# Kernel tuning notes

Hardware: AMD Instinct MI355X
Metric: run time of the kernel (lower is better)

Reference implementation:

```python
import jax, jax.numpy as jnp
import numpy as np

N = 100_000      # nodes
E = 1_600_000    # edges (before self loops)
IN, HID, OUT, H = 128, 32, 40, 4
NEG_SLOPE = 0.2  # PyG GATConv default


def setup_inputs() -> dict:
    key = jax.random.key(0)
    ks = jax.random.split(key, 10)
    s = 0.1  # small init scale (glorot-like)
    return {
        "x": jax.random.normal(ks[0], (N, IN), jnp.float32),
        "edge_index": jax.random.randint(ks[1], (2, E), 0, N, dtype=jnp.int32),
        "W1": jax.random.normal(ks[2], (IN, H * HID), jnp.float32) * s,
        "att_src1": jax.random.normal(ks[3], (H, HID), jnp.float32) * s,
        "att_dst1": jax.random.normal(ks[4], (H, HID), jnp.float32) * s,
        "b1": jnp.zeros((H * HID,), jnp.float32),
        "W2": jax.random.normal(ks[5], (H * HID, H * OUT), jnp.float32) * s,
        "att_src2": jax.random.normal(ks[6], (H, OUT), jnp.float32) * s,
        "att_dst2": jax.random.normal(ks[7], (H, OUT), jnp.float32) * s,
        "b2": jnp.zeros((OUT,), jnp.float32),
    }


def gat_layer(x, src, dst, W, a_src, a_dst, b, concat):
    """PyG-style GATConv: edge (src -> dst), softmax over incoming edges per dst."""
    Hh, C = a_src.shape
    h = (x @ W).reshape(-1, Hh, C)                      # [N, H, C]
    s_src = jnp.einsum('nhc,hc->nh', h, a_src)           # [N, H]
    s_dst = jnp.einsum('nhc,hc->nh', h, a_dst)           # [N, H]
    e = jax.nn.leaky_relu(s_src[src] + s_dst[dst], NEG_SLOPE)  # [E', H]
    m = jax.ops.segment_max(e, dst, num_segments=N)      # per-dst max for stability
    p = jnp.exp(e - m[dst])
    z = jax.ops.segment_sum(p, dst, num_segments=N)
    alpha = p / z[dst]                                    # segment softmax [E', H]
    out = jax.ops.segment_sum(alpha[:, :, None] * h[src], dst, num_segments=N)  # [N,H,C]
    out = out.reshape(-1, Hh * C) if concat else out.mean(axis=1)
    return out + b


def reference(x, edge_index, W1, att_src1, att_dst1, b1, W2, att_src2, att_dst2, b2):
    loops = jnp.arange(N, dtype=edge_index.dtype)        # PyG add_self_loops=True
    src = jnp.concatenate([edge_index[0], loops])
    dst = jnp.concatenate([edge_index[1], loops])
    h = jax.nn.elu(gat_layer(x, src, dst, W1, att_src1, att_dst1, b1, concat=True))
    h = gat_layer(h, src, dst, W2, att_src2, att_dst2, b2, concat=False)
    return jax.nn.log_softmax(h, axis=1)
```

## Files before the change

kernel.cpp:

```cpp
#include <hip/hip_runtime.h>
#include <hip/hip_bf16.h>

#define N_NODES 100000
#define M_PAD   100096
#define N_EDGES 1600000
#define E_TOT   (N_EDGES + N_NODES)
#define NEG_SLOPE 0.2f

#define G_NODES 128
#define BUCKETS ((N_NODES + G_NODES - 1) / G_NODES)
#define REP 512
#define SLICE ((E_TOT + REP - 1) / REP)
#define GB1 (M_PAD / 128)
#define CVTW_ELEMS (128 * 128 + 128 * 160)
#define CVTW_BLOCKS ((CVTW_ELEMS + 255) / 256)

typedef __attribute__((ext_vector_type(8))) short s16x8;
typedef __attribute__((ext_vector_type(4))) float f32x4;
typedef __attribute__((ext_vector_type(2))) float f32x2;

__device__ __forceinline__ float lo16(unsigned u) { return __uint_as_float(u << 16); }
__device__ __forceinline__ float hi16(unsigned u) { return __uint_as_float(u & 0xffff0000u); }

__device__ __forceinline__ short f2bf(float f) {
    __hip_bfloat16 b = __float2bfloat16(f);
    return *(short*)&b;
}


__device__ void slice_count_body(const int* __restrict__ ei, int* __restrict__ cnt, int r) {
    __shared__ int h[BUCKETS];
    for (int i = threadIdx.x; i < BUCKETS; i += 256) h[i] = 0;
    __syncthreads();
    int lo = r * SLICE, hi = min(lo + SLICE, E_TOT);
    for (int e = lo + threadIdx.x; e < hi; e += 256) {
        int d = (e < N_EDGES) ? ei[N_EDGES + e] : e - N_EDGES;
        atomicAdd(&h[d >> 7], 1);
    }
    __syncthreads();
    for (int i = threadIdx.x; i < BUCKETS; i += 256)
        cnt[(size_t)r * BUCKETS + i] = h[i];
}

__device__ void col_scan256_body(int* __restrict__ cnt, int* __restrict__ bsum, int b) {
    __shared__ int lds[256];
    int tid = threadIdx.x;
    int v0 = cnt[(size_t)(2 * tid) * BUCKETS + b];
    int v1 = cnt[(size_t)(2 * tid + 1) * BUCKETS + b];
    int s = v0 + v1;
    lds[tid] = s;
    __syncthreads();
    for (int off = 1; off < 256; off <<= 1) {
        int t = (tid >= off) ? lds[tid - off] : 0;
        __syncthreads();
        lds[tid] += t;
        __syncthreads();
    }
    int excl = lds[tid] - s;
    cnt[(size_t)(2 * tid) * BUCKETS + b]     = excl;
    cnt[(size_t)(2 * tid + 1) * BUCKETS + b] = excl + v0;
    if (tid == 255) bsum[b] = lds[255];
}

__device__ void bucket_scan_body(const int* __restrict__ bsum, int* __restrict__ boff) {
    __shared__ int lds[1024];
    int tid = threadIdx.x;
    int v = (tid < BUCKETS) ? bsum[tid] : 0;
    lds[tid] = v;
    __syncthreads();
    for (int off = 1; off < 1024; off <<= 1) {
        int t = (tid >= off) ? lds[tid - off] : 0;
        __syncthreads();
        lds[tid] += t;
        __syncthreads();
    }
    if (tid < BUCKETS) boff[tid] = lds[tid] - v;
    if (tid == 0) boff[BUCKETS] = E_TOT;
}

__global__ __launch_bounds__(256) void bucket_scatter_kernel(const int* __restrict__ ei,
                                                             const int* __restrict__ colx,
                                                             const int* __restrict__ boff,
                                                             int* __restrict__ tmp) {
    __shared__ int lcur[BUCKETS];
    int r = blockIdx.x;
    for (int i = threadIdx.x; i < BUCKETS; i += 256)
        lcur[i] = boff[i] + colx[(size_t)r * BUCKETS + i];
    __syncthreads();
    int lo = r * SLICE, hi = min(lo + SLICE, E_TOT);
    for (int e = lo + threadIdx.x; e < hi; e += 256) {
        int s, d;
        if (e < N_EDGES) { s = ei[e]; d = ei[N_EDGES + e]; }
        else             { s = d = e - N_EDGES; }
        int pos = atomicAdd(&lcur[d >> 7], 1);
        tmp[pos] = (s << 7) | (d & (G_NODES - 1));
    }
}

__global__ __launch_bounds__(256) void bucket_build_kernel(const int* __restrict__ tmp,
                                                           const int* __restrict__ boff,
                                                           int* __restrict__ rowptr,
                                                           int* __restrict__ csr) {
    __shared__ int hcnt[G_NODES];
    __shared__ int hoff[G_NODES];
    int b = blockIdx.x;
    int base = boff[b], cnt = boff[b + 1] - base;
    int tid = threadIdx.x;
    if (tid < G_NODES) hcnt[tid] = 0;
    __syncthreads();
    for (int i = tid; i < cnt; i += 256)
        atomicAdd(&hcnt[tmp[base + i] & (G_NODES - 1)], 1);
    __syncthreads();
    if (tid < G_NODES) hoff[tid] = hcnt[tid];
    __syncthreads();
    for (int off = 1; off < G_NODES; off <<= 1) {
        int t = (tid < G_NODES && tid >= off) ? hoff[tid - off] : 0;
        __syncthreads();
        if (tid < G_NODES) hoff[tid] += t;
        __syncthreads();
    }
    if (tid < G_NODES) {
        int excl = hoff[tid] - hcnt[tid];
        int node = b * G_NODES + tid;
        if (node < N_NODES) rowptr[node] = base + excl;
        hcnt[tid] = excl;
    }
    __syncthreads();
    for (int i = tid; i < cnt; i += 256) {
        int v = tmp[base + i];
        int pos = base + atomicAdd(&hcnt[v & (G_NODES - 1)], 1);
        csr[pos] = v >> 7;
    }
    if (b == 0 && tid < 8) csr[E_TOT + tid] = 0;
    if (b == 0 && tid == 0) rowptr[N_NODES] = E_TOT;
}


__device__ void cvt_w_body(const float* __restrict__ W1, __hip_bfloat16* __restrict__ W1t,
                           const float* __restrict__ W2, __hip_bfloat16* __restrict__ W2t,
                           int idx) {
    if (idx < 128 * 128) {
        int k = idx >> 7, n = idx & 127;
        W1t[n * 128 + k] = __float2bfloat16(W1[idx]);
    } else if (idx < CVTW_ELEMS) {
        int i = idx - 128 * 128;
        int k = i / 160, n = i - k * 160;
        W2t[n * 128 + k] = __float2bfloat16(W2[i]);
    }
}

__device__ void gemm1_body(const float* __restrict__ A, const __hip_bfloat16* __restrict__ Bt,
                           unsigned char* __restrict__ Cq, int bid) {
    constexpr int NCOLS = 128;
    constexpr int CG = NCOLS / 32;
    int wid = threadIdx.x >> 6;
    int lane = threadIdx.x & 63;
    int wr = wid >> 1, wc = wid & 1;
    int l15 = lane & 15, lk = lane >> 4;

    s16x8 bfrag[CG][4];
    #pragma unroll
    for (int cg = 0; cg < CG; ++cg) {
        int col = wc * (NCOLS / 2) + cg * 16 + l15;
        #pragma unroll
        for (int ks = 0; ks < 4; ++ks)
            bfrag[cg][ks] = *(const s16x8*)&Bt[col * 128 + ks * 32 + lk * 8];
    }
    int rowblk = bid * 128;
    #pragma unroll
    for (int st = 0; st < 4; ++st) {
        int rbase = rowblk + st * 32 + wr * 16;
        int row = rbase + l15;
        bool ok = row < N_NODES;
        s16x8 afrag[4];
        #pragma unroll
        for (int ks = 0; ks < 4; ++ks) {
            if (ok) {
                float4 a0 = *(const float4*)&A[(size_t)row * 128 + ks * 32 + lk * 8];
                float4 a1 = *(const float4*)&A[(size_t)row * 128 + ks * 32 + lk * 8 + 4];
                s16x8 af;
                af[0] = f2bf(a0.x); af[1] = f2bf(a0.y); af[2] = f2bf(a0.z); af[3] = f2bf(a0.w);
                af[4] = f2bf(a1.x); af[5] = f2bf(a1.y); af[6] = f2bf(a1.z); af[7] = f2bf(a1.w);
                afrag[ks] = af;
            } else {
                afrag[ks] = (s16x8){0,0,0,0,0,0,0,0};
            }
        }
        f32x4 acc[CG];
        #pragma unroll
        for (int cg = 0; cg < CG; ++cg) acc[cg] = (f32x4){0.f, 0.f, 0.f, 0.f};
        #pragma unroll
        for (int ks = 0; ks < 4; ++ks) {
            #pragma unroll
            for (int cg = 0; cg < CG; ++cg)
                acc[cg] = __builtin_amdgcn_mfma_f32_16x16x32_bf16(afrag[ks], bfrag[cg][ks], acc[cg], 0, 0, 0);
        }
        #pragma unroll
        for (int cg = 0; cg < CG; ++cg) {
            int c = wc * (NCOLS / 2) + cg * 16 + l15;
            unsigned w01 = __builtin_amdgcn_cvt_pk_fp8_f32(acc[cg][0], acc[cg][1], 0, false);
            unsigned w23 = __builtin_amdgcn_cvt_pk_fp8_f32(acc[cg][2], acc[cg][3], 0, false);
            size_t base = (size_t)(rbase + lk * 4) * NCOLS + c;
            Cq[base]             = (unsigned char)(w01 & 0xff);
            Cq[base + NCOLS]     = (unsigned char)((w01 >> 8) & 0xff);
            Cq[base + 2 * NCOLS] = (unsigned char)(w23 & 0xff);
            Cq[base + 3 * NCOLS] = (unsigned char)((w23 >> 8) & 0xff);
        }
    }
}

template<int NCOLS>
__global__ __launch_bounds__(256) void mfma_gemm_kernel(const __hip_bfloat16* __restrict__ A,
                                                        const __hip_bfloat16* __restrict__ Bt,
                                                        unsigned char* __restrict__ Cq) {
    constexpr int CG = NCOLS / 32;
    int wid = threadIdx.x >> 6;
    int lane = threadIdx.x & 63;
    int wr = wid >> 1, wc = wid & 1;
    int l15 = lane & 15, lk = lane >> 4;

    s16x8 bfrag[CG][4];
    #pragma unroll
    for (int cg = 0; cg < CG; ++cg) {
        int col = wc * (NCOLS / 2) + cg * 16 + l15;
        #pragma unroll
        for (int ks = 0; ks < 4; ++ks)
            bfrag[cg][ks] = *(const s16x8*)&Bt[col * 128 + ks * 32 + lk * 8];
    }
    int rowblk = blockIdx.x * 128;
    #pragma unroll
    for (int st = 0; st < 4; ++st) {
        int rbase = rowblk + st * 32 + wr * 16;
        s16x8 afrag[4];
        #pragma unroll
        for (int ks = 0; ks < 4; ++ks)
            afrag[ks] = *(const s16x8*)&A[(size_t)(rbase + l15) * 128 + ks * 32 + lk * 8];
        f32x4 acc[CG];
        #pragma unroll
        for (int cg = 0; cg < CG; ++cg) acc[cg] = (f32x4){0.f, 0.f, 0.f, 0.f};
        #pragma unroll
        for (int ks = 0; ks < 4; ++ks) {
            #pragma unroll
            for (int cg = 0; cg < CG; ++cg)
                acc[cg] = __builtin_amdgcn_mfma_f32_16x16x32_bf16(afrag[ks], bfrag[cg][ks], acc[cg], 0, 0, 0);
        }
        #pragma unroll
        for (int cg = 0; cg < CG; ++cg) {
            int c = wc * (NCOLS / 2) + cg * 16 + l15;
            unsigned w01 = __builtin_amdgcn_cvt_pk_fp8_f32(acc[cg][0], acc[cg][1], 0, false);
            unsigned w23 = __builtin_amdgcn_cvt_pk_fp8_f32(acc[cg][2], acc[cg][3], 0, false);
            size_t base = (size_t)(rbase + lk * 4) * NCOLS + c;
            Cq[base]             = (unsigned char)(w01 & 0xff);
            Cq[base + NCOLS]     = (unsigned char)((w01 >> 8) & 0xff);
            Cq[base + 2 * NCOLS] = (unsigned char)(w23 & 0xff);
            Cq[base + 3 * NCOLS] = (unsigned char)((w23 >> 8) & 0xff);
        }
    }
}


template<int C, int J>
__device__ void score_body(const unsigned char* __restrict__ hq,
                           const float* __restrict__ att_src,
                           const float* __restrict__ att_dst,
                           float* __restrict__ s_src, float* __restrict__ s_dst, int idx) {
    if (idx >= N_NODES * 4) return;
    int node = idx >> 2, hd = idx & 3;
    const unsigned char* hp = hq + (size_t)node * J + hd * C;
    const float* as = att_src + hd * C;
    const float* ad = att_dst + hd * C;
    float ss = 0.f, sd = 0.f;
    #pragma unroll
    for (int c8 = 0; c8 < C / 8; ++c8) {
        uint2 u = *(const uint2*)&hp[c8 * 8];
        f32x2 v0 = __builtin_amdgcn_cvt_pk_f32_fp8(u.x, false);
        f32x2 v1 = __builtin_amdgcn_cvt_pk_f32_fp8(u.x, true);
        f32x2 v2 = __builtin_amdgcn_cvt_pk_f32_fp8(u.y, false);
        f32x2 v3 = __builtin_amdgcn_cvt_pk_f32_fp8(u.y, true);
        int c = c8 * 8;
        ss += v0.x * as[c]     + v0.y * as[c + 1] + v1.x * as[c + 2] + v1.y * as[c + 3]
            + v2.x * as[c + 4] + v2.y * as[c + 5] + v3.x * as[c + 6] + v3.y * as[c + 7];
        sd += v0.x * ad[c]     + v0.y * ad[c + 1] + v1.x * ad[c + 2] + v1.y * ad[c + 3]
            + v2.x * ad[c + 4] + v2.y * ad[c + 5] + v3.x * ad[c + 6] + v3.y * ad[c + 7];
    }
    s_src[idx] = ss;
    s_dst[idx] = sd;
}

template<int C, int J>
__global__ void score_fp8_kernel(const unsigned char* __restrict__ hq,
                                 const float* __restrict__ att_src,
                                 const float* __restrict__ att_dst,
                                 float* __restrict__ s_src, float* __restrict__ s_dst) {
    score_body<C, J>(hq, att_src, att_dst, s_src, s_dst,
                     blockIdx.x * blockDim.x + threadIdx.x);
}


__global__ __launch_bounds__(256) void k0_slice_cvtw(const int* __restrict__ ei,
                                                     int* __restrict__ cnt,
                                                     const float* __restrict__ W1,
                                                     __hip_bfloat16* __restrict__ W1t,
                                                     const float* __restrict__ W2,
                                                     __hip_bfloat16* __restrict__ W2t) {
    if (blockIdx.x < REP) { slice_count_body(ei, cnt, blockIdx.x); return; }
    cvt_w_body(W1, W1t, W2, W2t, (blockIdx.x - REP) * 256 + threadIdx.x);
}

__global__ __launch_bounds__(256) void k1_colscan_gemm1(int* __restrict__ cnt,
                                                        int* __restrict__ bsum,
                                                        const float* __restrict__ A,
                                                        const __hip_bfloat16* __restrict__ Bt,
                                                        unsigned char* __restrict__ Cq) {
    if (blockIdx.x < BUCKETS) { col_scan256_body(cnt, bsum, blockIdx.x); return; }
    gemm1_body(A, Bt, Cq, blockIdx.x - BUCKETS);
}

__global__ __launch_bounds__(1024) void k2_bscan_score1(const int* __restrict__ bsum,
                                                        int* __restrict__ boff,
                                                        const unsigned char* __restrict__ h1q,
                                                        const float* __restrict__ as1,
                                                        const float* __restrict__ ad1,
                                                        float* __restrict__ s_src1,
                                                        float* __restrict__ s_dst1) {
    if (blockIdx.x == 0) { bucket_scan_body(bsum, boff); return; }
    score_body<32, 128>(h1q, as1, ad1, s_src1, s_dst1,
                        (blockIdx.x - 1) * 1024 + threadIdx.x);
}


__global__ __launch_bounds__(256) void agg1_kernel(
        const unsigned char* __restrict__ h1q, const float* __restrict__ s_src,
        const float* __restrict__ s_dst, const int* __restrict__ rowptr,
        const int* __restrict__ csr, const float* __restrict__ b1,
        __hip_bfloat16* __restrict__ out1) {
    int d = blockIdx.x * 4 + (threadIdx.x >> 6);
    if (d >= N_NODES) return;
    int lane = threadIdx.x & 63;
    int c0 = lane * 2;
    int hd = lane >> 4;
    int bp = hd << 2;
    int eg = (lane >> 2) & 7;
    float sdall = s_dst[d * 4 + (lane & 3)];
    f32x2 acc = {0.f, 0.f};
    float z = 0.f;
    int beg = __builtin_amdgcn_readfirstlane(rowptr[d]);
    int end = __builtin_amdgcn_readfirstlane(rowptr[d + 1]);
    for (int j = beg; j < end; j += 8) {
        int cnt = end - j;
        int se = csr[min(j + eg, end - 1)];
        float ee = s_src[(size_t)se * 4 + (lane & 3)] + sdall;
        ee = fmaxf(ee, NEG_SLOPE * ee);
        float qv = (eg < cnt) ? __expf(ee) : 0.f;
        int qbits = __float_as_int(qv);
        #pragma unroll
        for (int t = 0; t < 8; ++t) {
            float q = __int_as_float(__builtin_amdgcn_ds_bpermute(bp + t * 16, qbits));
            int s = __builtin_amdgcn_readfirstlane(csr[min(j + t, end - 1)]);
            const unsigned char* row = h1q + (size_t)s * 128;
            unsigned u = *(const unsigned short*)&row[c0];
            f32x2 v = __builtin_amdgcn_cvt_pk_f32_fp8(u, false);
            f32x2 qq = {q, q};
            acc += qq * v;
            z += q;
        }
    }
    float invz = 1.0f / z;
    float vx = acc.x * invz + b1[c0];
    float vy = acc.y * invz + b1[c0 + 1];
    vx = vx > 0.f ? vx : __expf(vx) - 1.0f;
    vy = vy > 0.f ? vy : __expf(vy) - 1.0f;
    __hip_bfloat162 o;
    o.x = __float2bfloat16(vx);
    o.y = __float2bfloat16(vy);
    *(__hip_bfloat162*)&out1[(size_t)d * 128 + c0] = o;
}

__global__ __launch_bounds__(256) void agg2_kernel(
        const unsigned char* __restrict__ h2q, const float* __restrict__ s_src,
        const float* __restrict__ s_dst, const int* __restrict__ rowptr,
        const int* __restrict__ csr, const float* __restrict__ b2,
        float* __restrict__ out) {
    int d = blockIdx.x * 4 + (threadIdx.x >> 6);
    if (d >= N_NODES) return;
    int lane = threadIdx.x & 63;
    int ll = lane < 40 ? lane : 39;
    int hd = ll / 10;
    int bp = hd << 2;
    int eg = (lane >> 2) & 7;
    int voff = ll * 4;
    float sdall = s_dst[d * 4 + (lane & 3)];
    f32x2 acc01 = {0.f, 0.f}, acc23 = {0.f, 0.f};
    float z = 0.f;
    int beg = __builtin_amdgcn_readfirstlane(rowptr[d]);
    int end = __builtin_amdgcn_readfirstlane(rowptr[d + 1]);
    for (int j = beg; j < end; j += 8) {
        int cnt = end - j;
        int se = csr[min(j + eg, end - 1)];
        float ee = s_src[(size_t)se * 4 + (lane & 3)] + sdall;
        ee = fmaxf(ee, NEG_SLOPE * ee);
        float qv = (eg < cnt) ? __expf(ee) : 0.f;
        int qbits = __float_as_int(qv);
        #pragma unroll
        for (int t = 0; t < 8; ++t) {
            float q = __int_as_float(__builtin_amdgcn_ds_bpermute(bp + t * 16, qbits));
            int s = __builtin_amdgcn_readfirstlane(csr[min(j + t, end - 1)]);
            const unsigned char* row = h2q + (size_t)s * 160;
            unsigned u = *(const unsigned*)&row[voff];
            f32x2 v01 = __builtin_amdgcn_cvt_pk_f32_fp8(u, false);
            f32x2 v23 = __builtin_amdgcn_cvt_pk_f32_fp8(u, true);
            f32x2 qq = {q, q};
            acc01 += qq * v01;
            acc23 += qq * v23;
            z += q;
        }
    }
    float invz = 1.0f / z;
    float rx = acc01.x * invz, ry = acc01.y * invz;
    float rz = acc23.x * invz, rw = acc23.y * invz;
    float sx = rx + __shfl(rx, lane + 10) + __shfl(rx, lane + 20) + __shfl(rx, lane + 30);
    float sy = ry + __shfl(ry, lane + 10) + __shfl(ry, lane + 20) + __shfl(ry, lane + 30);
    float sz = rz + __shfl(rz, lane + 10) + __shfl(rz, lane + 20) + __shfl(rz, lane + 30);
    float sw = rw + __shfl(rw, lane + 10) + __shfl(rw, lane + 20) + __shfl(rw, lane + 30);
    int lc = lane < 10 ? lane : 9;
    float4 bb = *(const float4*)&b2[lc * 4];
    bool own = lane < 10;
    float vx = own ? sx * 0.25f + bb.x : -1e30f;
    float vy = own ? sy * 0.25f + bb.y : -1e30f;
    float vz = own ? sz * 0.25f + bb.z : -1e30f;
    float vw = own ? sw * 0.25f + bb.w : -1e30f;
    float m = fmaxf(fmaxf(vx, vy), fmaxf(vz, vw));
    #pragma unroll
    for (int off = 1; off < 16; off <<= 1) m = fmaxf(m, __shfl_xor(m, off));
    float ssum = 0.f;
    if (own) {
        ssum = __expf(vx - m) + __expf(vy - m) + __expf(vz - m) + __expf(vw - m);
    }
    #pragma unroll
    for (int off = 1; off < 16; off <<= 1) ssum += __shfl_xor(ssum, off);
    float lse = m + __logf(ssum);
    if (own) {
        float4 o = {vx - lse, vy - lse, vz - lse, vw - lse};
        *(float4*)&out[(size_t)d * 40 + lane * 4] = o;
    }
}


extern "C" void kernel_launch(void* const* d_in, const int* in_sizes, int n_in,
                              void* d_out, int out_size, void* d_ws, size_t ws_size,
                              hipStream_t stream) {
    const float* x   = (const float*)d_in[0];
    const int*   ei  = (const int*)d_in[1];
    const float* W1  = (const float*)d_in[2];
    const float* as1 = (const float*)d_in[3];
    const float* ad1 = (const float*)d_in[4];
    const float* b1  = (const float*)d_in[5];
    const float* W2  = (const float*)d_in[6];
    const float* as2 = (const float*)d_in[7];
    const float* ad2 = (const float*)d_in[8];
    const float* b2  = (const float*)d_in[9];
    float* out = (float*)d_out;

    char* ws = (char*)d_ws;
    size_t off = 0;
    auto alloc = [&](size_t bytes) {
        void* p = ws + off;
        off += (bytes + 255) & ~(size_t)255;
        return p;
    };
    unsigned char*  h1q   = (unsigned char*)alloc((size_t)M_PAD * 128);
    unsigned char*  h2q   = (unsigned char*)alloc((size_t)M_PAD * 160);
    __hip_bfloat16* out1b = (__hip_bfloat16*)alloc((size_t)M_PAD * 128 * 2);
    __hip_bfloat16* W1t   = (__hip_bfloat16*)alloc((size_t)128 * 128 * 2);
    __hip_bfloat16* W2t   = (__hip_bfloat16*)alloc((size_t)160 * 128 * 2);
    float* s_src1  = (float*)alloc((size_t)N_NODES * 4 * 4);
    float* s_dst1  = (float*)alloc((size_t)N_NODES * 4 * 4);
    float* s_src2  = (float*)alloc((size_t)N_NODES * 4 * 4);
    float* s_dst2  = (float*)alloc((size_t)N_NODES * 4 * 4);
    int*   tmp     = (int*)alloc((size_t)E_TOT * 4);
    int*   rowptr  = (int*)alloc((size_t)(N_NODES + 1) * 4);
    int*   csr     = (int*)alloc((size_t)(E_TOT + 8) * 4);
    int*   cnt     = (int*)alloc((size_t)REP * BUCKETS * 4);
    int*   bsum    = (int*)alloc((size_t)BUCKETS * 4);
    int*   boff    = (int*)alloc((size_t)(BUCKETS + 1) * 4);

    k0_slice_cvtw<<<REP + CVTW_BLOCKS, 256, 0, stream>>>(ei, cnt, W1, W1t, W2, W2t);
    k1_colscan_gemm1<<<BUCKETS + GB1, 256, 0, stream>>>(cnt, bsum, x, W1t, h1q);
    k2_bscan_score1<<<1 + (N_NODES * 4 + 1023) / 1024, 1024, 0, stream>>>(
        bsum, boff, h1q, as1, ad1, s_src1, s_dst1);
    bucket_scatter_kernel<<<REP, 256, 0, stream>>>(ei, cnt, boff, tmp);
    bucket_build_kernel<<<BUCKETS, 256, 0, stream>>>(tmp, boff, rowptr, csr);

    agg1_kernel<<<(N_NODES + 3) / 4, 256, 0, stream>>>(h1q, s_src1, s_dst1, rowptr, csr, b1, out1b);

    mfma_gemm_kernel<160><<<GB1, 256, 0, stream>>>(out1b, W2t, h2q);
    score_fp8_kernel<40, 160><<<(N_NODES * 4 + 255) / 256, 256, 0, stream>>>(h2q, as2, ad2, s_src2, s_dst2);
    agg2_kernel<<<(N_NODES + 3) / 4, 256, 0, stream>>>(h2q, s_src2, s_dst2, rowptr, csr, b2, out);
}
```

Before: 242.1 us.

## Fuse attention score computation into GEMM epilogues for both GAT layers

Computes per-node, per-head source and destination attention scores directly from the fp32 MFMA accumulators inside both GEMM kernels, using lane shuffles. This removes the separate score kernels and their re-read of the fp8 feature matrices. The bucket scan moves into its own single-block launch. The GEMM epilogue gains shuffle reductions and scattered small stores, and scores now come from unquantized accumulators.

Result: faster. 234.8 us (median of 2 runs) (-3.0%).

```diff
diff --git a/kernel.cpp b/kernel.cpp
--- a/kernel.cpp
+++ b/kernel.cpp
@@ -62,7 +62,8 @@
     if (tid == 255) bsum[b] = lds[255];
 }
 
-__device__ void bucket_scan_body(const int* __restrict__ bsum, int* __restrict__ boff) {
+__global__ __launch_bounds__(1024) void bucket_scan_kernel(const int* __restrict__ bsum,
+                                                           int* __restrict__ boff) {
     __shared__ int lds[1024];
     int tid = threadIdx.x;
     int v = (tid < BUCKETS) ? bsum[tid] : 0;
@@ -149,8 +150,47 @@
     }
 }
 
+
+template<int NCOLS>
+__device__ __forceinline__ void score_epilogue(const f32x4* acc, int rbase, int wc,
+                                               int l15, int lk,
+                                               const float* __restrict__ as,
+                                               const float* __restrict__ ad,
+                                               float* __restrict__ s_src,
+                                               float* __restrict__ s_dst) {
+    constexpr int CG = NCOLS / 32;
+    constexpr int HEADW = NCOLS / 4;
+    #pragma unroll
+    for (int j = 0; j < 4; ++j) {
+        float pa = 0.f, pb = 0.f, qa = 0.f, qb = 0.f;
+        #pragma unroll
+        for (int cg = 0; cg < CG; ++cg) {
+            int c = wc * (NCOLS / 2) + cg * 16 + l15;
+            float v = acc[cg][j];
+            float ws = as[c], wd = ad[c];
+            if (c >= (wc * 2 + 1) * HEADW) { pb += v * ws; qb += v * wd; }
+            else                           { pa += v * ws; qa += v * wd; }
+        }
+        #pragma unroll
+        for (int off = 1; off < 16; off <<= 1) {
+            pa += __shfl_xor(pa, off); pb += __shfl_xor(pb, off);
+            qa += __shfl_xor(qa, off); qb += __shfl_xor(qb, off);
+        }
+        int row = rbase + lk * 4 + j;
+        if (l15 == 0 && row < N_NODES) {
+            int ha = wc * 2;
+            s_src[row * 4 + ha]     = pa;
+            s_src[row * 4 + ha + 1] = pb;
+            s_dst[row * 4 + ha]     = qa;
+            s_dst[row * 4 + ha + 1] = qb;
+        }
+    }
+}
+
 __device__ void gemm1_body(const float* __restrict__ A, const __hip_bfloat16* __restrict__ Bt,
-                           unsigned char* __restrict__ Cq, int bid) {
+                           unsigned char* __restrict__ Cq,
+                           const float* __restrict__ as, const float* __restrict__ ad,
+                           float* __restrict__ s_src, float* __restrict__ s_dst, int bid) {
     constexpr int NCOLS = 128;
     constexpr int CG = NCOLS / 32;
     int wid = threadIdx.x >> 6;
@@ -206,13 +246,18 @@
             Cq[base + 2 * NCOLS] = (unsigned char)(w23 & 0xff);
             Cq[base + 3 * NCOLS] = (unsigned char)((w23 >> 8) & 0xff);
         }
+        score_epilogue<NCOLS>(acc, rbase, wc, l15, lk, as, ad, s_src, s_dst);
     }
 }
 
 template<int NCOLS>
-__global__ __launch_bounds__(256) void mfma_gemm_kernel(const __hip_bfloat16* __restrict__ A,
-                                                        const __hip_bfloat16* __restrict__ Bt,
-                                                        unsigned char* __restrict__ Cq) {
+__global__ __launch_bounds__(256) void mfma_gemm_score_kernel(const __hip_bfloat16* __restrict__ A,
+                                                              const __hip_bfloat16* __restrict__ Bt,
+                                                              unsigned char* __restrict__ Cq,
+                                                              const float* __restrict__ as,
+                                                              const float* __restrict__ ad,
+                                                              float* __restrict__ s_src,
+                                                              float* __restrict__ s_dst) {
     constexpr int CG = NCOLS / 32;
     int wid = threadIdx.x >> 6;
     int lane = threadIdx.x & 63;
@@ -255,45 +300,8 @@
             Cq[base + 2 * NCOLS] = (unsigned char)(w23 & 0xff);
             Cq[base + 3 * NCOLS] = (unsigned char)((w23 >> 8) & 0xff);
         }
-    }
-}
-
-
-template<int C, int J>
-__device__ void score_body(const unsigned char* __restrict__ hq,
-                           const float* __restrict__ att_src,
-                           const float* __restrict__ att_dst,
-                           float* __restrict__ s_src, float* __restrict__ s_dst, int idx) {
-    if (idx >= N_NODES * 4) return;
-    int node = idx >> 2, hd = idx & 3;
-    const unsigned char* hp = hq + (size_t)node * J + hd * C;
-    const float* as = att_src + hd * C;
-    const float* ad = att_dst + hd * C;
-    float ss = 0.f, sd = 0.f;
-    #pragma unroll
-    for (int c8 = 0; c8 < C / 8; ++c8) {
-        uint2 u = *(const uint2*)&hp[c8 * 8];
-        f32x2 v0 = __builtin_amdgcn_cvt_pk_f32_fp8(u.x, false);
-        f32x2 v1 = __builtin_amdgcn_cvt_pk_f32_fp8(u.x, true);
-        f32x2 v2 = __builtin_amdgcn_cvt_pk_f32_fp8(u.y, false);
-        f32x2 v3 = __builtin_amdgcn_cvt_pk_f32_fp8(u.y, true);
-        int c = c8 * 8;
-        ss += v0.x * as[c]     + v0.y * as[c + 1] + v1.x * as[c + 2] + v1.y * as[c + 3]
-            + v2.x * as[c + 4] + v2.y * as[c + 5] + v3.x * as[c + 6] + v3.y * as[c + 7];
-        sd += v0.x * ad[c]     + v0.y * ad[c + 1] + v1.x * ad[c + 2] + v1.y * ad[c + 3]
-            + v2.x * ad[c + 4] + v2.y * ad[c + 5] + v3.x * ad[c + 6] + v3.y * ad[c + 7];
-    }
-    s_src[idx] = ss;
-    s_dst[idx] = sd;
-}
-
-template<int C, int J>
-__global__ void score_fp8_kernel(const unsigned char* __restrict__ hq,
-                                 const float* __restrict__ att_src,
-                                 const float* __restrict__ att_dst,
-                                 float* __restrict__ s_src, float* __restrict__ s_dst) {
-    score_body<C, J>(hq, att_src, att_dst, s_src, s_dst,
-                     blockIdx.x * blockDim.x + threadIdx.x);
+        score_epilogue<NCOLS>(acc, rbase, wc, l15, lk, as, ad, s_src, s_dst);
+    }
 }
 
 
@@ -311,21 +319,13 @@
                                                         int* __restrict__ bsum,
                                                         const float* __restrict__ A,
                                                         const __hip_bfloat16* __restrict__ Bt,
-                                                        unsigned char* __restrict__ Cq) {
-    if (blockIdx.x < BUCKETS) { col_scan256_body(cnt, bsum, blockIdx.x); return; }
-    gemm1_body(A, Bt, Cq, blockIdx.x - BUCKETS);
-}
-
-__global__ __launch_bounds__(1024) void k2_bscan_score1(const int* __restrict__ bsum,
-                                                        int* __restrict__ boff,
-                                                        const unsigned char* __restrict__ h1q,
+                                                        unsigned char* __restrict__ Cq,
                                                         const float* __restrict__ as1,
                                                         const float* __restrict__ ad1,
                                                         float* __restrict__ s_src1,
                                                         float* __restrict__ s_dst1) {
-    if (blockIdx.x == 0) { bucket_scan_body(bsum, boff); return; }
-    score_body<32, 128>(h1q, as1, ad1, s_src1, s_dst1,
-                        (blockIdx.x - 1) * 1024 + threadIdx.x);
+    if (blockIdx.x < BUCKETS) { col_scan256_body(cnt, bsum, blockIdx.x); return; }
+    gemm1_body(A, Bt, Cq, as1, ad1, s_src1, s_dst1, blockIdx.x - BUCKETS);
 }
 
 
@@ -485,15 +485,15 @@
     int*   boff    = (int*)alloc((size_t)(BUCKETS + 1) * 4);
 
     k0_slice_cvtw<<<REP + CVTW_BLOCKS, 256, 0, stream>>>(ei, cnt, W1, W1t, W2, W2t);
-    k1_colscan_gemm1<<<BUCKETS + GB1, 256, 0, stream>>>(cnt, bsum, x, W1t, h1q);
-    k2_bscan_score1<<<1 + (N_NODES * 4 + 1023) / 1024, 1024, 0, stream>>>(
-        bsum, boff, h1q, as1, ad1, s_src1, s_dst1);
+    k1_colscan_gemm1<<<BUCKETS + GB1, 256, 0, stream>>>(cnt, bsum, x, W1t, h1q,
+                                                        as1, ad1, s_src1, s_dst1);
+    bucket_scan_kernel<<<1, 1024, 0, stream>>>(bsum, boff);
     bucket_scatter_kernel<<<REP, 256, 0, stream>>>(ei, cnt, boff, tmp);
     bucket_build_kernel<<<BUCKETS, 256, 0, stream>>>(tmp, boff, rowptr, csr);
 
     agg1_kernel<<<(N_NODES + 3) / 4, 256, 0, stream>>>(h1q, s_src1, s_dst1, rowptr, csr, b1, out1b);
 
-    mfma_gemm_kernel<160><<<GB1, 256, 0, stream>>>(out1b, W2t, h2q);
-    score_fp8_kernel<40, 160><<<(N_NODES * 4 + 255) / 256, 256, 0, stream>>>(h2q, as2, ad2, s_src2, s_dst2);
+    mfma_gemm_score_kernel<160><<<GB1, 256, 0, stream>>>(out1b, W2t, h2q,
+                                                         as2, ad2, s_src2, s_dst2);
     agg2_kernel<<<(N_NODES + 3) / 4, 256, 0, stream>>>(h2q, s_src2, s_dst2, rowptr, csr, b2, out);
 }
```
